# Optimization experiments

Measured on AMD Instinct MI355X. Metric: run time of the kernel, lower is better.

The kernel has to match this reference:

```python
import jax, jax.numpy as jnp
import numpy as np


def setup_inputs() -> dict:
    key = jax.random.key(0)
    kq, kk, kv, km = jax.random.split(key, 4)
    B, H, S, D = 2, 16, 2048, 64
    Q = jax.random.normal(kq, (B, H, S, D), dtype=jnp.float32)
    K = jax.random.normal(kk, (B, H, S, D), dtype=jnp.float32)
    V = jax.random.normal(kv, (B, H, S, D), dtype=jnp.float32)
    mask = jax.random.randint(km, (B, 1, S, S), 0, 2).astype(jnp.bool_)
    return {"Q": Q, "K": K, "V": V, "mask": mask}


def reference(Q, K, V, mask):
    # scores: [B, H, Sq, Sk]
    scores = jnp.einsum("bhqd,bhkd->bhqk", Q, K)
    neg = jnp.finfo(scores.dtype).min
    # Faithful to original: mask fill happens BEFORE the sqrt(d) scaling.
    scores = jnp.where(mask, neg, scores)
    inv_sqrt_d = 1.0 / jnp.sqrt(jnp.asarray(Q.shape[-1], dtype=scores.dtype))
    attn = jax.nn.softmax(scores * inv_sqrt_d, axis=-1)
    return jnp.einsum("bhqk,bhkd->bhqd", attn, V)
```

## Files before the change

### kernel.cpp

```cpp
#include <hip/hip_runtime.h>
#include <stdint.h>


#define SQ 2048
#define DH 64

using bf16x8  = __attribute__((ext_vector_type(8)))  __bf16;
using f32x4   = __attribute__((ext_vector_type(4)))  float;
using ushort8 = __attribute__((ext_vector_type(8)))  unsigned short;
using ushort4v= __attribute__((ext_vector_type(4)))  unsigned short;

static __device__ __forceinline__ unsigned short f2bf(float f) {
    union { float f; uint32_t u; } c; c.f = f;
    return (unsigned short)((c.u + 0x8000u) >> 16);
}

static __device__ __forceinline__ int swz(int row, int col) {
    return row * 64 + ((((col >> 3) ^ (row & 7))) << 3) + (col & 7);
}

static __device__ __forceinline__ f32x4 mfma16(bf16x8 a, bf16x8 b, f32x4 c) {
    return __builtin_amdgcn_mfma_f32_16x16x32_bf16(a, b, c, 0, 0, 0);
}

__global__ void pack_mask_kernel(const int* __restrict__ mask,
                                 unsigned long long* __restrict__ words, int nwords) {
    int gid = blockIdx.x * blockDim.x + threadIdx.x;
    int w = gid >> 6;
    int l = gid & 63;
    if (w < nwords) {
        int mv = mask[(size_t)w * 64 + l];
        unsigned long long b = __ballot(mv != 0);
        if (l == 0) words[w] = b;
    }
}

__global__ __launch_bounds__(256, 4)
void attn_kernel(const float* __restrict__ Q, const float* __restrict__ K,
                 const float* __restrict__ V,
                 const unsigned long long* __restrict__ Mw,
                 float* __restrict__ out) {
    __shared__ __align__(16) unsigned short Ks[64 * 64];
    __shared__ __align__(16) unsigned short Vt[64 * 64];
    __shared__ __align__(16) unsigned short Ps[4 * 16 * 64];

    const int tid  = threadIdx.x;
    const int w    = tid >> 6;
    const int l    = tid & 63;
    const int quad = l >> 4;
    const int c16  = l & 15;
    const int bx = blockIdx.x;
    const int hh = bx & 15;
    const int b  = (bx >> 4) & 1;
    const int qt = bx >> 5;

    const size_t bh = (size_t)b * 16 + hh;
    const float* Qp = Q + bh * SQ * DH;
    const float* Kp = K + bh * SQ * DH;
    const float* Vp = V + bh * SQ * DH;
    const int qw = qt * 64 + 16 * w;
    const unsigned long long* Mq = Mw + ((size_t)b * SQ + qw + quad * 4) * (SQ / 64);

    bf16x8 qf[2];
    {
        const float* qr = Qp + (size_t)(qw + c16) * DH;
        #pragma unroll
        for (int c = 0; c < 2; ++c) {
            int d0 = 32 * c + 8 * quad;
            float4 a  = *(const float4*)(qr + d0);
            float4 b4 = *(const float4*)(qr + d0 + 4);
            ushort8 t;
            t[0]=f2bf(a.x);  t[1]=f2bf(a.y);  t[2]=f2bf(a.z);  t[3]=f2bf(a.w);
            t[4]=f2bf(b4.x); t[5]=f2bf(b4.y); t[6]=f2bf(b4.z); t[7]=f2bf(b4.w);
            qf[c] = __builtin_bit_cast(bf16x8, t);
        }
    }

    f32x4 o[4];
    float lsum[4];
    #pragma unroll
    for (int i = 0; i < 4; ++i) { o[i] = (f32x4)(0.f); lsum[i] = 0.f; }

    unsigned short* Pw = Ps + w * (16 * 64);
    const int xg = (c16 & 7);

    for (int t = 0; t < 32; ++t) {
        const int kt0 = t * 64;

        unsigned long long mws[4];
        #pragma unroll
        for (int r = 0; r < 4; ++r) mws[r] = Mq[(size_t)r * (SQ / 64) + t];

        __syncthreads();

        #pragma unroll
        for (int i = 0; i < 4; ++i) {
            int idx = tid + 256 * i;
            int key = idx >> 4;
            int d0  = (idx & 15) << 2;
            float4 kv = *(const float4*)(Kp + (size_t)(kt0 + key) * DH + d0);
            ushort4v tt;
            tt[0]=f2bf(kv.x); tt[1]=f2bf(kv.y); tt[2]=f2bf(kv.z); tt[3]=f2bf(kv.w);
            *(ushort4v*)&Ks[swz(key, d0)] = tt;
        }
        #pragma unroll
        for (int p = 0; p < 4; ++p) {
            int k0l = 16 * w + 4 * p;
            const float* vb = Vp + (size_t)(kt0 + k0l) * DH + l;
            float x0 = vb[0], x1 = vb[DH], x2 = vb[2*DH], x3 = vb[3*DH];
            ushort4v tt;
            tt[0]=f2bf(x0); tt[1]=f2bf(x1); tt[2]=f2bf(x2); tt[3]=f2bf(x3);
            *(ushort4v*)&Vt[swz(l, k0l)] = tt;
        }
        __syncthreads();

        f32x4 s[4];
        #pragma unroll
        for (int i = 0; i < 4; ++i) s[i] = (f32x4)(0.f);
        #pragma unroll
        for (int c = 0; c < 2; ++c) {
            int g = ((4 * c + quad) ^ xg) << 3;
            #pragma unroll
            for (int nb = 0; nb < 4; ++nb) {
                bf16x8 kb = __builtin_bit_cast(bf16x8,
                    *(const ushort8*)&Ks[(c16 + 16 * nb) * 64 + g]);
                s[nb] = mfma16(qf[c], kb, s[nb]);
            }
        }

        #pragma unroll
        for (int r = 0; r < 4; ++r) {
            int row = quad * 4 + r;
            unsigned lo = (unsigned)mws[r];
            unsigned hi = (unsigned)(mws[r] >> 32);
            #pragma unroll
            for (int nb = 0; nb < 4; ++nb) {
                float e = __builtin_amdgcn_exp2f(fmaf(s[nb][r], 0.18033688f, -5.7707802f));
                unsigned bits = (nb & 2) ? hi : lo;
                unsigned bit  = 1u << (c16 + 16 * (nb & 1));
                float pv = (bits & bit) ? 0.0f : e;
                lsum[r] += pv;
                Pw[swz(row, c16 + 16 * nb)] = f2bf(pv);
            }
        }

        bf16x8 pa[2];
        #pragma unroll
        for (int c = 0; c < 2; ++c)
            pa[c] = __builtin_bit_cast(bf16x8,
                *(const ushort8*)&Pw[c16 * 64 + (((4 * c + quad) ^ xg) << 3)]);
        #pragma unroll
        for (int c = 0; c < 2; ++c) {
            int g = ((4 * c + quad) ^ xg) << 3;
            #pragma unroll
            for (int db = 0; db < 4; ++db) {
                bf16x8 vb = __builtin_bit_cast(bf16x8,
                    *(const ushort8*)&Vt[(c16 + 16 * db) * 64 + g]);
                o[db] = mfma16(pa[c], vb, o[db]);
            }
        }
    }

    #pragma unroll
    for (int r = 0; r < 4; ++r) {
        float v = lsum[r];
        v += __shfl_xor(v, 1, 64);
        v += __shfl_xor(v, 2, 64);
        v += __shfl_xor(v, 4, 64);
        v += __shfl_xor(v, 8, 64);
        float rinv = 1.0f / v;
        float* op = out + (bh * SQ + (size_t)(qw + quad * 4 + r)) * DH + c16;
        #pragma unroll
        for (int db = 0; db < 4; ++db) op[16 * db] = o[db][r] * rinv;
    }
}

extern "C" void kernel_launch(void* const* d_in, const int* in_sizes, int n_in,
                              void* d_out, int out_size, void* d_ws, size_t ws_size,
                              hipStream_t stream) {
    const float* Q    = (const float*)d_in[0];
    const float* K    = (const float*)d_in[1];
    const float* V    = (const float*)d_in[2];
    const int*   mask = (const int*)d_in[3];
    float* out = (float*)d_out;
    unsigned long long* mwords = (unsigned long long*)d_ws;

    const int nwords = 2 * SQ * (SQ / 64);
    pack_mask_kernel<<<dim3((nwords * 64) / 256), dim3(256), 0, stream>>>(mask, mwords, nwords);
    attn_kernel<<<dim3(1024), dim3(256), 0, stream>>>(Q, K, V, mwords, out);
}
```

Measured before the change: 193.0 us.

## Pre-convert K/V to bf16 and double-buffer tiles via async global-to-LDS loads

Adds pre-pass kernels that convert K to bf16 and transpose V into bf16 in workspace. The attention kernel then streams pre-swizzled tiles straight into double-buffered LDS with global_load_lds, prefetching the next tile and its mask words while computing the current one. This removes repeated per-block fp32 loads and conversions, since each K/V tile is otherwise reconverted by every q-tile block. It also cuts one barrier per iteration. In exchange it adds two extra launches, workspace traffic and twice the LDS, which may reduce occupancy.

```diff
diff --git a/kernel.cpp b/kernel.cpp
--- a/kernel.cpp
+++ b/kernel.cpp
@@ -21,6 +21,12 @@
 
 static __device__ __forceinline__ f32x4 mfma16(bf16x8 a, bf16x8 b, f32x4 c) {
     return __builtin_amdgcn_mfma_f32_16x16x32_bf16(a, b, c, 0, 0, 0);
+}
+
+static __device__ __forceinline__ void gload16(const void* g, void* l) {
+    __builtin_amdgcn_global_load_lds(
+        (const __attribute__((address_space(1))) void*)g,
+        (__attribute__((address_space(3))) void*)l, 16, 0, 0);
 }
 
 __global__ void pack_mask_kernel(const int* __restrict__ mask,
@@ -35,13 +41,55 @@
     }
 }
 
+__global__ void cvt_bf16_kernel(const float* __restrict__ src,
+                                unsigned short* __restrict__ dst) {
+    int gid = blockIdx.x * blockDim.x + threadIdx.x;
+    float4 v = ((const float4*)src)[gid];
+    ushort4v t;
+    t[0] = f2bf(v.x); t[1] = f2bf(v.y); t[2] = f2bf(v.z); t[3] = f2bf(v.w);
+    ((ushort4v*)dst)[gid] = t;
+}
+
+__global__ __launch_bounds__(256)
+void vtrans_kernel(const float* __restrict__ V, unsigned short* __restrict__ Vt) {
+    __shared__ unsigned short tl[64][66];
+    const int tid = threadIdx.x;
+    const int kt  = blockIdx.x & 31;
+    const size_t bh = blockIdx.x >> 5;
+    const float* vp = V + (bh * SQ + (size_t)kt * 64) * DH;
+    #pragma unroll
+    for (int i = 0; i < 4; ++i) {
+        int idx = tid + 256 * i;
+        int key = idx >> 4;
+        int dc  = (idx & 15) * 4;
+        float4 v = *(const float4*)(vp + (size_t)key * DH + dc);
+        tl[key][dc + 0] = f2bf(v.x);
+        tl[key][dc + 1] = f2bf(v.y);
+        tl[key][dc + 2] = f2bf(v.z);
+        tl[key][dc + 3] = f2bf(v.w);
+    }
+    __syncthreads();
+    unsigned short* op = Vt + bh * DH * SQ + (size_t)kt * 64;
+    #pragma unroll
+    for (int i = 0; i < 4; ++i) {
+        int idx = tid + 256 * i;
+        int d  = idx >> 4;
+        int kc = (idx & 15) * 4;
+        ushort4v t;
+        t[0] = tl[kc + 0][d]; t[1] = tl[kc + 1][d];
+        t[2] = tl[kc + 2][d]; t[3] = tl[kc + 3][d];
+        *(ushort4v*)(op + (size_t)d * SQ + kc) = t;
+    }
+}
+
 __global__ __launch_bounds__(256, 4)
-void attn_kernel(const float* __restrict__ Q, const float* __restrict__ K,
-                 const float* __restrict__ V,
+void attn_kernel(const float* __restrict__ Q,
+                 const unsigned short* __restrict__ Kb,
+                 const unsigned short* __restrict__ Vtg,
                  const unsigned long long* __restrict__ Mw,
                  float* __restrict__ out) {
-    __shared__ __align__(16) unsigned short Ks[64 * 64];
-    __shared__ __align__(16) unsigned short Vt[64 * 64];
+    __shared__ __align__(16) unsigned short Ks[2][64 * 64];
+    __shared__ __align__(16) unsigned short Vs[2][64 * 64];
     __shared__ __align__(16) unsigned short Ps[4 * 16 * 64];
 
     const int tid  = threadIdx.x;
@@ -56,10 +104,19 @@
 
     const size_t bh = (size_t)b * 16 + hh;
     const float* Qp = Q + bh * SQ * DH;
-    const float* Kp = K + bh * SQ * DH;
-    const float* Vp = V + bh * SQ * DH;
     const int qw = qt * 64 + 16 * w;
     const unsigned long long* Mq = Mw + ((size_t)b * SQ + qw + quad * 4) * (SQ / 64);
+
+    const int s0 = (2 * w) * 64 + l;
+    const int s1 = (2 * w + 1) * 64 + l;
+    const int r0 = s0 >> 3, g0 = s0 & 7;
+    const int r1 = s1 >> 3, g1 = s1 & 7;
+    const char* Kg = (const char*)(Kb  + bh * (size_t)SQ * DH);
+    const char* Vg = (const char*)(Vtg + bh * (size_t)DH * SQ);
+    const char* kSrc0 = Kg + r0 * 128  + ((g0 ^ (r0 & 7)) << 4);
+    const char* kSrc1 = Kg + r1 * 128  + ((g1 ^ (r1 & 7)) << 4);
+    const char* vSrc0 = Vg + r0 * 4096 + ((g0 ^ (r0 & 7)) << 4);
+    const char* vSrc1 = Vg + r1 * 4096 + ((g1 ^ (r1 & 7)) << 4);
 
     bf16x8 qf[2];
     {
@@ -84,35 +141,33 @@
     unsigned short* Pw = Ps + w * (16 * 64);
     const int xg = (c16 & 7);
 
+    unsigned long long mws[4];
+    #pragma unroll
+    for (int r = 0; r < 4; ++r) mws[r] = Mq[(size_t)r * (SQ / 64)];
+
+    gload16(kSrc0, &Ks[0][(2 * w) * 512]);
+    gload16(kSrc1, &Ks[0][(2 * w + 1) * 512]);
+    gload16(vSrc0, &Vs[0][(2 * w) * 512]);
+    gload16(vSrc1, &Vs[0][(2 * w + 1) * 512]);
+    kSrc0 += 8192; kSrc1 += 8192; vSrc0 += 128; vSrc1 += 128;
+    __syncthreads();
+
     for (int t = 0; t < 32; ++t) {
-        const int kt0 = t * 64;
-
-        unsigned long long mws[4];
-        #pragma unroll
-        for (int r = 0; r < 4; ++r) mws[r] = Mq[(size_t)r * (SQ / 64) + t];
-
-        __syncthreads();
-
-        #pragma unroll
-        for (int i = 0; i < 4; ++i) {
-            int idx = tid + 256 * i;
-            int key = idx >> 4;
-            int d0  = (idx & 15) << 2;
-            float4 kv = *(const float4*)(Kp + (size_t)(kt0 + key) * DH + d0);
-            ushort4v tt;
-            tt[0]=f2bf(kv.x); tt[1]=f2bf(kv.y); tt[2]=f2bf(kv.z); tt[3]=f2bf(kv.w);
-            *(ushort4v*)&Ks[swz(key, d0)] = tt;
-        }
-        #pragma unroll
-        for (int p = 0; p < 4; ++p) {
-            int k0l = 16 * w + 4 * p;
-            const float* vb = Vp + (size_t)(kt0 + k0l) * DH + l;
-            float x0 = vb[0], x1 = vb[DH], x2 = vb[2*DH], x3 = vb[3*DH];
-            ushort4v tt;
-            tt[0]=f2bf(x0); tt[1]=f2bf(x1); tt[2]=f2bf(x2); tt[3]=f2bf(x3);
-            *(ushort4v*)&Vt[swz(l, k0l)] = tt;
-        }
-        __syncthreads();
+        const int cur = t & 1;
+
+        unsigned long long nmws[4];
+        if (t < 31) {
+            gload16(kSrc0, &Ks[cur ^ 1][(2 * w) * 512]);
+            gload16(kSrc1, &Ks[cur ^ 1][(2 * w + 1) * 512]);
+            gload16(vSrc0, &Vs[cur ^ 1][(2 * w) * 512]);
+            gload16(vSrc1, &Vs[cur ^ 1][(2 * w + 1) * 512]);
+            kSrc0 += 8192; kSrc1 += 8192; vSrc0 += 128; vSrc1 += 128;
+            #pragma unroll
+            for (int r = 0; r < 4; ++r) nmws[r] = Mq[(size_t)r * (SQ / 64) + (t + 1)];
+        }
+
+        const unsigned short* Kc = Ks[cur];
+        const unsigned short* Vc = Vs[cur];
 
         f32x4 s[4];
         #pragma unroll
@@ -123,7 +178,7 @@
             #pragma unroll
             for (int nb = 0; nb < 4; ++nb) {
                 bf16x8 kb = __builtin_bit_cast(bf16x8,
-                    *(const ushort8*)&Ks[(c16 + 16 * nb) * 64 + g]);
+                    *(const ushort8*)&Kc[(c16 + 16 * nb) * 64 + g]);
                 s[nb] = mfma16(qf[c], kb, s[nb]);
             }
         }
@@ -155,9 +210,15 @@
             #pragma unroll
             for (int db = 0; db < 4; ++db) {
                 bf16x8 vb = __builtin_bit_cast(bf16x8,
-                    *(const ushort8*)&Vt[(c16 + 16 * db) * 64 + g]);
+                    *(const ushort8*)&Vc[(c16 + 16 * db) * 64 + g]);
                 o[db] = mfma16(pa[c], vb, o[db]);
             }
+        }
+
+        __syncthreads();
+        if (t < 31) {
+            #pragma unroll
+            for (int r = 0; r < 4; ++r) mws[r] = nmws[r];
         }
     }
 
@@ -183,9 +244,15 @@
     const float* V    = (const float*)d_in[2];
     const int*   mask = (const int*)d_in[3];
     float* out = (float*)d_out;
-    unsigned long long* mwords = (unsigned long long*)d_ws;
+
+    char* ws = (char*)d_ws;
+    unsigned long long* mwords = (unsigned long long*)ws;
+    unsigned short* Kb = (unsigned short*)(ws + (1 << 20));
+    unsigned short* Vt = (unsigned short*)(ws + (1 << 20) + (8 << 20));
 
     const int nwords = 2 * SQ * (SQ / 64);
     pack_mask_kernel<<<dim3((nwords * 64) / 256), dim3(256), 0, stream>>>(mask, mwords, nwords);
-    attn_kernel<<<dim3(1024), dim3(256), 0, stream>>>(Q, K, V, mwords, out);
-}
+    cvt_bf16_kernel<<<dim3(4096), dim3(256), 0, stream>>>(K, Kb);
+    vtrans_kernel<<<dim3(1024), dim3(256), 0, stream>>>(V, Vt);
+    attn_kernel<<<dim3(1024), dim3(256), 0, stream>>>(Q, Kb, Vt, mwords, out);
+}
```

Result: faster. 189.2 us (-2.0%).
